# Kernel optimization log

Measured on AMD Instinct MI355X. Metric: run time of the kernel, lower is better.

## Reference

```python
import jax, jax.numpy as jnp
import numpy as np

B, NC, N, D_N, ALPHA = 8, 32, 128, 64, 4
HS, HM, HMOD = 128, 128, 64
MOD_IN = 2 * D_N + 5          # 133
MOD_OUT = N * N + N           # 16512


def setup_inputs() -> dict:
    key = jax.random.key(0)
    ks = jax.random.split(key, 16)
    f = jax.random.normal
    eye = jnp.eye(N, dtype=jnp.float32)
    return {
        "x": f(ks[0], (B, NC * D_N), jnp.float32),
        "h": f(ks[1], (B, NC, N, D_N), jnp.float32) * 0.01,
        "msg": f(ks[2], (B, NC, N, D_N), jnp.float32) * 0.1,
        "W": jnp.abs(f(ks[3], (B, NC, N, N), jnp.float32)) * 0.05 * (1.0 - eye),
        "decay_logit": f(ks[4], (B, NC, N), jnp.float32) * 0.1,
        "readout_drift": f(ks[5], (B, NC, 1), jnp.float32) * 0.1,
        "s_mem_live": f(ks[6], (B,), jnp.float32) * 0.1,
        "s_mem_ema_fast": f(ks[7], (B,), jnp.float32) * 0.1,
        "neuron_id": f(ks[8], (NC, N, D_N), jnp.float32) * 0.02,
        "state_w1": f(ks[9], (HS, 2 * D_N), jnp.float32) / np.sqrt(2 * D_N),
        "state_b1": jnp.zeros((HS,), jnp.float32),
        "state_w2": f(ks[10], (D_N, HS), jnp.float32) * 0.1 / np.sqrt(HS),
        "state_b2": jnp.zeros((D_N,), jnp.float32),
        "msg_w1": f(ks[11], (HM, D_N), jnp.float32) / np.sqrt(D_N),
        "msg_b1": jnp.zeros((HM,), jnp.float32),
        "msg_w2": f(ks[12], (D_N, HM), jnp.float32) * 0.1 / np.sqrt(HM),
        "msg_b2": jnp.zeros((D_N,), jnp.float32),
        "inject_w": f(ks[13], (NC, ALPHA * D_N, D_N), jnp.float32) / np.sqrt(D_N),
        "inject_b": jnp.zeros((NC, ALPHA * D_N), jnp.float32),
        "mod_w1": f(ks[14], (NC, MOD_IN, HMOD), jnp.float32) / np.sqrt(MOD_IN),
        "mod_b1": jnp.zeros((NC, HMOD), jnp.float32),
        "mod_w2": f(ks[15], (NC, HMOD, MOD_OUT), jnp.float32) * 0.01 / np.sqrt(HMOD),
        "mod_b2": jnp.zeros((NC, MOD_OUT), jnp.float32),
    }


def reference(x, h, msg, W, decay_logit, readout_drift, s_mem_live, s_mem_ema_fast,
              neuron_id, state_w1, state_b1, state_w2, state_b2,
              msg_w1, msg_b1, msg_w2, msg_b2, inject_w, inject_b,
              mod_w1, mod_b1, mod_w2, mod_b2):
    # --- message receive: dense per-cell adjacency matmul ---
    decay = jax.nn.sigmoid(decay_logit)[..., None]            # (B,NC,N,1)
    received = jnp.einsum('bcnm,bcmd->bcnd', W, msg)          # (B,NC,N,D_n)
    # --- inject external input into the alpha input-port neurons ---
    cell = x.reshape(B, NC, D_N)
    inj = jnp.einsum('bci,coi->bco', cell, inject_w) + inject_b   # (B,NC,alpha*D_n)
    received = received.at[:, :, :ALPHA].add(inj.reshape(B, NC, ALPHA, D_N))
    # --- state MLP with split first layer (avoids cat([received, h])) ---
    w1_recv, w1_h = state_w1[:, :D_N], state_w1[:, D_N:]
    hidden = jnp.tanh(jnp.einsum('bcnd,hd->bcnh', received, w1_recv)
                      + jnp.einsum('bcnd,hd->bcnh', h, w1_h) + state_b1)
    cand = jnp.tanh(jnp.einsum('bcnh,dh->bcnd', hidden, state_w2) + state_b2)
    h_new = decay * h + (1.0 - decay) * cand
    # --- emit message ---
    mh = jnp.tanh(jnp.einsum('bcnd,hd->bcnh', h_new, msg_w1) + msg_b1)
    msg_new = jnp.tanh(jnp.einsum('bcnh,dh->bcnd', mh, msg_w2) + msg_b2) + neuron_id[None]
    # --- readout from alpha output-port neurons ---
    readout = msg_new[:, :, ALPHA:2 * ALPHA].sum(axis=2) * (ALPHA ** -0.5)  # (B,NC,D_n)
    readout_flat = readout.reshape(B, NC * D_N)
    # --- per-cell modulator (stats -> tanh MLP -> delta_W, delta_decay) ---
    h_mean = h_new.mean(axis=2)                               # (B,NC,D_n)
    msg_mean = msg_new.mean(axis=2)
    W_stats = jnp.abs(W).mean(axis=-1).mean(axis=2, keepdims=True)  # (B,NC,1)
    decay_mean = decay_logit.mean(axis=2, keepdims=True)
    s1 = jnp.broadcast_to(s_mem_live[:, None, None], (B, NC, 1))
    s2 = jnp.broadcast_to(s_mem_ema_fast[:, None, None], (B, NC, 1))
    mod_input = jnp.concatenate([h_mean, msg_mean, W_stats, decay_mean,
                                 readout_drift, s1, s2], axis=-1)      # (B,NC,2*D_n+5)
    hid = jnp.tanh(jnp.einsum('bci,cih->bch', mod_input, mod_w1) + mod_b1)
    outm = jnp.einsum('bch,cho->bco', hid, mod_w2) + mod_b2            # (B,NC,N*N+N)
    delta_W = outm[..., :N * N].reshape(B, NC, N, N)
    delta_decay = outm[..., N * N:]
    eye = jnp.eye(N, dtype=W.dtype)
    W_new = (W + delta_W) * (1.0 - eye)   # additive modulation, no self-edges
    decay_new = decay_logit + delta_decay
    return readout_flat, h_new, msg_new, W_new, decay_new
```

## Files before the change

kernel.cpp:

```cpp
#include <hip/hip_runtime.h>
#include <math.h>


#define OUT_RO   0u
#define OUT_H    16384u
#define OUT_MSG  2113536u
#define OUT_W    4210688u
#define OUT_DEC  8404992u

#define TID ((int)threadIdx.x)

__device__ __forceinline__ float tanh_f(float v){ return tanhf(v); }

__global__ __launch_bounds__(256, 1)
void k1_cell(const float* __restrict__ x,
             const float* __restrict__ hg,
             const float* __restrict__ msgg,
             const float* __restrict__ Wg,
             const float* __restrict__ decay_logit,
             const float* __restrict__ readout_drift,
             const float* __restrict__ s_mem_live,
             const float* __restrict__ s_mem_ema_fast,
             const float* __restrict__ neuron_id,
             const float* __restrict__ state_w1,
             const float* __restrict__ state_b1,
             const float* __restrict__ state_w2,
             const float* __restrict__ state_b2,
             const float* __restrict__ msg_w1,
             const float* __restrict__ msg_b1,
             const float* __restrict__ msg_w2,
             const float* __restrict__ msg_b2,
             const float* __restrict__ inject_w,
             const float* __restrict__ inject_b,
             const float* __restrict__ mod_w1,
             const float* __restrict__ mod_b1,
             float* __restrict__ out,
             float* __restrict__ hid_ws)
{
    __shared__ __align__(16) float sD[128*132];
    __shared__ __align__(16) float sA[128*68];
    __shared__ __align__(16) float sB[128*68];
    __shared__ __align__(16) float s_b1[128];
    __shared__ __align__(16) float s_mb1[128];
    __shared__ __align__(16) float s_b2[64];
    __shared__ __align__(16) float s_mb2[64];
    __shared__ __align__(16) float s_cell[64];
    __shared__ __align__(16) float s_dlog[128];
    __shared__ __align__(16) float s_dec[128];
    __shared__ __align__(16) float s_modin[136];
    __shared__ __align__(16) float s_scr[16*68];
    __shared__ float s_wpart[4];

    const int bid = blockIdx.x;
    const int b   = bid >> 5;
    const int c   = bid & 31;
    const int ty  = TID >> 4;
    const int tx  = TID & 15;
    const int d4  = tx * 4;

    float wabs = 0.f;
    {
        const float4* src = (const float4*)(Wg + (size_t)bid * 16384);
        #pragma unroll
        for (int it = 0; it < 16; ++it) {
            int f4i = TID + it * 256;
            float4 v = src[f4i];
            int n = f4i >> 5, k = (f4i & 31) << 2;
            *(float4*)&sD[n*132 + k] = v;
            wabs += fabsf(v.x) + fabsf(v.y) + fabsf(v.z) + fabsf(v.w);
        }
    }
    {
        const float4* src = (const float4*)(msgg + (size_t)bid * 8192);
        #pragma unroll
        for (int it = 0; it < 8; ++it) {
            int f4i = TID + it * 256;
            float4 v = src[f4i];
            int n = f4i >> 4, d = (f4i & 15) << 2;
            *(float4*)&sA[n*68 + d] = v;
        }
    }
    {
        const float4* src = (const float4*)(hg + (size_t)bid * 8192);
        #pragma unroll
        for (int it = 0; it < 8; ++it) {
            int f4i = TID + it * 256;
            float4 v = src[f4i];
            int n = f4i >> 4, d = (f4i & 15) << 2;
            *(float4*)&sB[n*68 + d] = v;
        }
    }
    if (TID < 128) {
        s_b1[TID]  = state_b1[TID];
        s_mb1[TID] = msg_b1[TID];
        float dl = decay_logit[(size_t)bid*128 + TID];
        s_dlog[TID] = dl;
        s_dec[TID]  = 1.f / (1.f + expf(-dl));
    }
    if (TID < 64) {
        s_b2[TID]   = state_b2[TID];
        s_mb2[TID]  = msg_b2[TID];
        s_cell[TID] = x[(size_t)b*2048 + c*64 + TID];
    }
    #pragma unroll
    for (int off = 32; off > 0; off >>= 1) wabs += __shfl_down(wabs, off);
    if ((TID & 63) == 0) s_wpart[TID >> 6] = wabs;

    __syncthreads();

    float4 acc[8];
    #pragma unroll
    for (int i = 0; i < 8; ++i) acc[i] = make_float4(0.f,0.f,0.f,0.f);
    #pragma unroll 4
    for (int k = 0; k < 128; ++k) {
        float4 m4 = *(const float4*)&sA[k*68 + d4];
        #pragma unroll
        for (int i = 0; i < 8; ++i) {
            float w = sD[(ty + 16*i)*132 + k];
            acc[i].x += w * m4.x; acc[i].y += w * m4.y;
            acc[i].z += w * m4.z; acc[i].w += w * m4.w;
        }
    }
    __syncthreads();

    #pragma unroll
    for (int i = 0; i < 8; ++i)
        *(float4*)&sA[(ty + 16*i)*68 + d4] = acc[i];
    {
        const float4* src = (const float4*)state_w1;
        #pragma unroll
        for (int it = 0; it < 16; ++it) {
            int f4i = TID + it * 256;
            float4 v = src[f4i];
            int n = f4i >> 5, k = (f4i & 31) << 2;
            *(float4*)&sD[n*132 + k] = v;
        }
    }
    if (TID == 0) {
        float ws_ = (s_wpart[0] + s_wpart[1] + s_wpart[2] + s_wpart[3]) * (1.f/16384.f);
        float ds = 0.f;
        for (int n = 0; n < 128; ++n) ds += s_dlog[n];
        s_modin[128] = ws_;
        s_modin[129] = ds * (1.f/128.f);
        s_modin[130] = readout_drift[bid];
        s_modin[131] = s_mem_live[b];
        s_modin[132] = s_mem_ema_fast[b];
    }
    __syncthreads();

    {
        int o = TID;
        float s = inject_b[(size_t)c*256 + o];
        const float4* iw = (const float4*)(inject_w + (size_t)c*16384 + (size_t)o*64);
        #pragma unroll 4
        for (int q = 0; q < 16; ++q) {
            float4 w4 = iw[q];
            float4 cl = *(const float4*)&s_cell[q*4];
            s += w4.x*cl.x + w4.y*cl.y + w4.z*cl.z + w4.w*cl.w;
        }
        sA[(o >> 6)*68 + (o & 63)] += s;
    }
    __syncthreads();

    {
        float acc2[8][8];
        #pragma unroll
        for (int i = 0; i < 8; ++i)
            #pragma unroll
            for (int j = 0; j < 8; ++j) acc2[i][j] = 0.f;
        #pragma unroll 2
        for (int k = 0; k < 64; ++k) {
            float rv[8], hv[8], wr[8], wh[8];
            #pragma unroll
            for (int i = 0; i < 8; ++i) {
                int n = ty + 16*i;
                rv[i] = sA[n*68 + k];
                hv[i] = sB[n*68 + k];
            }
            #pragma unroll
            for (int j = 0; j < 8; ++j) {
                int hh = tx + 16*j;
                wr[j] = sD[hh*132 + k];
                wh[j] = sD[hh*132 + 64 + k];
            }
            #pragma unroll
            for (int i = 0; i < 8; ++i)
                #pragma unroll
                for (int j = 0; j < 8; ++j)
                    acc2[i][j] += rv[i]*wr[j] + hv[i]*wh[j];
        }
        __syncthreads();
        #pragma unroll
        for (int i = 0; i < 8; ++i)
            #pragma unroll
            for (int j = 0; j < 8; ++j)
                sD[(ty + 16*i)*132 + (tx + 16*j)] = tanh_f(acc2[i][j] + s_b1[tx + 16*j]);
    }
    {
        const float4* src = (const float4*)state_w2;
        #pragma unroll
        for (int it = 0; it < 8; ++it) {
            int f4i = TID + it * 256;
            float4 v = src[f4i];
            int d = f4i >> 5, hh = (f4i & 31) << 2;
            sA[(hh+0)*68 + d] = v.x;
            sA[(hh+1)*68 + d] = v.y;
            sA[(hh+2)*68 + d] = v.z;
            sA[(hh+3)*68 + d] = v.w;
        }
    }
    __syncthreads();

    {
        #pragma unroll
        for (int i = 0; i < 8; ++i) acc[i] = make_float4(0.f,0.f,0.f,0.f);
        #pragma unroll 4
        for (int k = 0; k < 128; ++k) {
            float4 w4 = *(const float4*)&sA[k*68 + d4];
            #pragma unroll
            for (int i = 0; i < 8; ++i) {
                float hv = sD[(ty + 16*i)*132 + k];
                acc[i].x += hv * w4.x; acc[i].y += hv * w4.y;
                acc[i].z += hv * w4.z; acc[i].w += hv * w4.w;
            }
        }
        float4 b2v = *(const float4*)&s_b2[d4];
        float4 hpart = make_float4(0.f,0.f,0.f,0.f);
        #pragma unroll
        for (int i = 0; i < 8; ++i) {
            int n = ty + 16*i;
            float dec = s_dec[n];
            float4 hold = *(const float4*)&sB[n*68 + d4];
            float4 hn;
            hn.x = dec*hold.x + (1.f-dec)*tanh_f(acc[i].x + b2v.x);
            hn.y = dec*hold.y + (1.f-dec)*tanh_f(acc[i].y + b2v.y);
            hn.z = dec*hold.z + (1.f-dec)*tanh_f(acc[i].z + b2v.z);
            hn.w = dec*hold.w + (1.f-dec)*tanh_f(acc[i].w + b2v.w);
            *(float4*)&sB[n*68 + d4] = hn;
            *(float4*)(out + OUT_H + (size_t)bid*8192 + n*64 + d4) = hn;
            hpart.x += hn.x; hpart.y += hn.y; hpart.z += hn.z; hpart.w += hn.w;
        }
        *(float4*)&s_scr[ty*68 + d4] = hpart;
    }
    __syncthreads();
    if (TID < 64) {
        float s = 0.f;
        #pragma unroll
        for (int t = 0; t < 16; ++t) s += s_scr[t*68 + TID];
        s_modin[TID] = s * (1.f/128.f);
    }
    {
        const float4* src = (const float4*)msg_w1;
        #pragma unroll
        for (int it = 0; it < 8; ++it) {
            int f4i = TID + it * 256;
            float4 v = src[f4i];
            int hh = f4i >> 4, d = (f4i & 15) << 2;
            *(float4*)&sA[hh*68 + d] = v;
        }
    }
    __syncthreads();

    {
        float acc2[8][8];
        #pragma unroll
        for (int i = 0; i < 8; ++i)
            #pragma unroll
            for (int j = 0; j < 8; ++j) acc2[i][j] = 0.f;
        #pragma unroll 2
        for (int k = 0; k < 64; ++k) {
            float hv[8], wv[8];
            #pragma unroll
            for (int i = 0; i < 8; ++i) hv[i] = sB[(ty + 16*i)*68 + k];
            #pragma unroll
            for (int j = 0; j < 8; ++j) wv[j] = sA[(tx + 16*j)*68 + k];
            #pragma unroll
            for (int i = 0; i < 8; ++i)
                #pragma unroll
                for (int j = 0; j < 8; ++j)
                    acc2[i][j] += hv[i]*wv[j];
        }
        __syncthreads();
        #pragma unroll
        for (int i = 0; i < 8; ++i)
            #pragma unroll
            for (int j = 0; j < 8; ++j)
                sD[(ty + 16*i)*132 + (tx + 16*j)] = tanh_f(acc2[i][j] + s_mb1[tx + 16*j]);
    }
    {
        const float4* src = (const float4*)msg_w2;
        #pragma unroll
        for (int it = 0; it < 8; ++it) {
            int f4i = TID + it * 256;
            float4 v = src[f4i];
            int d = f4i >> 5, hh = (f4i & 31) << 2;
            sA[(hh+0)*68 + d] = v.x;
            sA[(hh+1)*68 + d] = v.y;
            sA[(hh+2)*68 + d] = v.z;
            sA[(hh+3)*68 + d] = v.w;
        }
    }
    __syncthreads();

    {
        #pragma unroll
        for (int i = 0; i < 8; ++i) acc[i] = make_float4(0.f,0.f,0.f,0.f);
        #pragma unroll 4
        for (int k = 0; k < 128; ++k) {
            float4 w4 = *(const float4*)&sA[k*68 + d4];
            #pragma unroll
            for (int i = 0; i < 8; ++i) {
                float mv = sD[(ty + 16*i)*132 + k];
                acc[i].x += mv * w4.x; acc[i].y += mv * w4.y;
                acc[i].z += mv * w4.z; acc[i].w += mv * w4.w;
            }
        }
        float4 mb2 = *(const float4*)&s_mb2[d4];
        float4 mpart = make_float4(0.f,0.f,0.f,0.f);
        #pragma unroll
        for (int i = 0; i < 8; ++i) {
            int n = ty + 16*i;
            float4 nid = *(const float4*)(neuron_id + (size_t)c*8192 + n*64 + d4);
            float4 mn;
            mn.x = tanh_f(acc[i].x + mb2.x) + nid.x;
            mn.y = tanh_f(acc[i].y + mb2.y) + nid.y;
            mn.z = tanh_f(acc[i].z + mb2.z) + nid.z;
            mn.w = tanh_f(acc[i].w + mb2.w) + nid.w;
            *(float4*)&sB[n*68 + d4] = mn;
            *(float4*)(out + OUT_MSG + (size_t)bid*8192 + n*64 + d4) = mn;
            mpart.x += mn.x; mpart.y += mn.y; mpart.z += mn.z; mpart.w += mn.w;
        }
        *(float4*)&s_scr[ty*68 + d4] = mpart;
    }
    __syncthreads();
    if (TID < 64) {
        float s = 0.f;
        #pragma unroll
        for (int t = 0; t < 16; ++t) s += s_scr[t*68 + TID];
        s_modin[64 + TID] = s * (1.f/128.f);
        float r = (sB[4*68 + TID] + sB[5*68 + TID] + sB[6*68 + TID] + sB[7*68 + TID]) * 0.5f;
        out[OUT_RO + (size_t)b*2048 + c*64 + TID] = r;
    }
    __syncthreads();

    if (TID < 64) {
        int hh = TID;
        float a = mod_b1[(size_t)c*64 + hh];
        const float* w1p = mod_w1 + (size_t)c*8512 + hh;
        #pragma unroll 7
        for (int i = 0; i < 133; ++i)
            a += s_modin[i] * w1p[(size_t)i*64];
        hid_ws[(size_t)bid*64 + hh] = tanh_f(a);
    }
}

__global__ __launch_bounds__(512, 1)
void k2_wnew(const float* __restrict__ hid_ws,
             const float* __restrict__ mod_w2,
             const float* __restrict__ mod_b2,
             const float* __restrict__ Wg,
             const float* __restrict__ decay_logit,
             float* __restrict__ out)
{
    __shared__ float shid[512];
    const int c    = blockIdx.x >> 3;
    const int part = blockIdx.x & 7;

    shid[TID] = hid_ws[((size_t)((TID >> 6) * 32 + c))*64 + (TID & 63)];
    __syncthreads();

    for (int idx = TID; idx < 516; idx += 512) {
        int o = part * 2064 + idx * 4;
        float4 acc0[8];
        {
            float4 bv = *(const float4*)(mod_b2 + (size_t)c*16512 + o);
            #pragma unroll
            for (int bb = 0; bb < 8; ++bb) acc0[bb] = bv;
        }
        const float* w2p = mod_w2 + (size_t)c*1056768 + o;
        #pragma unroll 8
        for (int hh = 0; hh < 64; ++hh) {
            float4 w4 = *(const float4*)(w2p + (size_t)hh*16512);
            #pragma unroll
            for (int bb = 0; bb < 8; ++bb) {
                float hv = shid[bb*64 + hh];
                acc0[bb].x += hv * w4.x; acc0[bb].y += hv * w4.y;
                acc0[bb].z += hv * w4.z; acc0[bb].w += hv * w4.w;
            }
        }
        if (o < 16384) {
            int n = o >> 7, m = o & 127;
            #pragma unroll
            for (int bb = 0; bb < 8; ++bb) {
                size_t wof = ((size_t)(bb*32 + c) << 14) + o;
                float4 Wv = *(const float4*)(Wg + wof);
                float4 r;
                r.x = Wv.x + acc0[bb].x;
                r.y = Wv.y + acc0[bb].y;
                r.z = Wv.z + acc0[bb].z;
                r.w = Wv.w + acc0[bb].w;
                if (n == m)     r.x = 0.f;
                else if (n == m+1) r.y = 0.f;
                else if (n == m+2) r.z = 0.f;
                else if (n == m+3) r.w = 0.f;
                *(float4*)(out + OUT_W + wof) = r;
            }
        } else {
            int m = o - 16384;
            #pragma unroll
            for (int bb = 0; bb < 8; ++bb) {
                size_t dof = (size_t)(bb*32 + c)*128 + m;
                float4 dl = *(const float4*)(decay_logit + dof);
                float4 r;
                r.x = dl.x + acc0[bb].x;
                r.y = dl.y + acc0[bb].y;
                r.z = dl.z + acc0[bb].z;
                r.w = dl.w + acc0[bb].w;
                *(float4*)(out + OUT_DEC + dof) = r;
            }
        }
    }
}

extern "C" void kernel_launch(void* const* d_in, const int* in_sizes, int n_in,
                              void* d_out, int out_size, void* d_ws, size_t ws_size,
                              hipStream_t stream)
{
    (void)in_sizes; (void)n_in; (void)out_size; (void)ws_size;
    const float* x              = (const float*)d_in[0];
    const float* h              = (const float*)d_in[1];
    const float* msg            = (const float*)d_in[2];
    const float* W              = (const float*)d_in[3];
    const float* decay_logit    = (const float*)d_in[4];
    const float* readout_drift  = (const float*)d_in[5];
    const float* s_mem_live     = (const float*)d_in[6];
    const float* s_mem_ema_fast = (const float*)d_in[7];
    const float* neuron_id      = (const float*)d_in[8];
    const float* state_w1       = (const float*)d_in[9];
    const float* state_b1       = (const float*)d_in[10];
    const float* state_w2       = (const float*)d_in[11];
    const float* state_b2       = (const float*)d_in[12];
    const float* msg_w1         = (const float*)d_in[13];
    const float* msg_b1         = (const float*)d_in[14];
    const float* msg_w2         = (const float*)d_in[15];
    const float* msg_b2         = (const float*)d_in[16];
    const float* inject_w       = (const float*)d_in[17];
    const float* inject_b       = (const float*)d_in[18];
    const float* mod_w1         = (const float*)d_in[19];
    const float* mod_b1         = (const float*)d_in[20];
    const float* mod_w2         = (const float*)d_in[21];
    const float* mod_b2         = (const float*)d_in[22];

    float* out = (float*)d_out;
    float* ws  = (float*)d_ws;

    hipLaunchKernelGGL(k1_cell, dim3(256), dim3(256), 0, stream,
                       x, h, msg, W, decay_logit, readout_drift,
                       s_mem_live, s_mem_ema_fast, neuron_id,
                       state_w1, state_b1, state_w2, state_b2,
                       msg_w1, msg_b1, msg_w2, msg_b2,
                       inject_w, inject_b, mod_w1, mod_b1,
                       out, ws);

    hipLaunchKernelGGL(k2_wnew, dim3(256), dim3(512), 0, stream,
                       ws, mod_w2, mod_b2, W, decay_logit, out);
}
```

Before: 371.3 us.

## Rewrite cell kernel with bf16 MFMA matmuls and rebalance modulator grid

New measurement: 312.4 us. 15.9% less time.

```diff
diff --git a/kernel.cpp b/kernel.cpp
--- a/kernel.cpp
+++ b/kernel.cpp
@@ -8,11 +8,27 @@
 #define OUT_W    4210688u
 #define OUT_DEC  8404992u
 
-#define TID ((int)threadIdx.x)
-
-__device__ __forceinline__ float tanh_f(float v){ return tanhf(v); }
-
-__global__ __launch_bounds__(256, 1)
+typedef __bf16 bf16x8 __attribute__((ext_vector_type(8)));
+typedef float  f32x4  __attribute__((ext_vector_type(4)));
+
+__device__ __forceinline__ unsigned short bf16_rne(float f){
+    unsigned int u = __float_as_uint(f);
+    u += 0x7fffu + ((u >> 16) & 1u);
+    return (unsigned short)(u >> 16);
+}
+__device__ __forceinline__ float bf16_f(unsigned short s){
+    return __uint_as_float(((unsigned int)s) << 16);
+}
+__device__ __forceinline__ float tanh_fast(float x){
+    float e = __expf(2.f * x);
+    return 1.f - 2.f / (e + 1.f);
+}
+__device__ __forceinline__ bf16x8 frag(const unsigned short* p, int row, int stride, int kbyte){
+    return *(const bf16x8*)((const char*)(p + row * stride) + kbyte);
+}
+#define MFMA16(a, b, c) __builtin_amdgcn_mfma_f32_16x16x32_bf16(a, b, c, 0, 0, 0)
+
+__global__ __launch_bounds__(512)
 void k1_cell(const float* __restrict__ x,
              const float* __restrict__ hg,
              const float* __restrict__ msgg,
@@ -37,324 +53,374 @@
              float* __restrict__ out,
              float* __restrict__ hid_ws)
 {
-    __shared__ __align__(16) float sD[128*132];
-    __shared__ __align__(16) float sA[128*68];
-    __shared__ __align__(16) float sB[128*68];
-    __shared__ __align__(16) float s_b1[128];
-    __shared__ __align__(16) float s_mb1[128];
-    __shared__ __align__(16) float s_b2[64];
-    __shared__ __align__(16) float s_mb2[64];
-    __shared__ __align__(16) float s_cell[64];
-    __shared__ __align__(16) float s_dlog[128];
-    __shared__ __align__(16) float s_dec[128];
-    __shared__ __align__(16) float s_modin[136];
-    __shared__ __align__(16) float s_scr[16*68];
-    __shared__ float s_wpart[4];
-
-    const int bid = blockIdx.x;
-    const int b   = bid >> 5;
-    const int c   = bid & 31;
-    const int ty  = TID >> 4;
-    const int tx  = TID & 15;
-    const int d4  = tx * 4;
+    __shared__ __align__(16) unsigned short sW[128*136];
+    __shared__ __align__(16) unsigned short sM[64*136];
+    __shared__ __align__(16) unsigned short sR[128*72];
+    __shared__ __align__(16) unsigned short sH[128*72];
+    __shared__ __align__(16) float scrH[32*64];
+    __shared__ __align__(16) float scrM[32*64];
+    __shared__ __align__(16) float s_inj[256];
+    __shared__ float s_b1[128], s_mb1[128], s_b2[64], s_mb2[64];
+    __shared__ float s_cell[64], s_dlog[128], s_dec[128];
+    __shared__ float s_modin[136];
+    __shared__ float s_wpart[8];
+
+    const int tid  = (int)threadIdx.x;
+    const int bid  = (int)blockIdx.x;
+    const int b    = bid >> 5, c = bid & 31;
+    const int wid  = tid >> 6, lane = tid & 63;
+    const int q    = lane >> 4, r16 = lane & 15;
+    const int wm   = wid >> 1, wn = wid & 1;
+    const int ar   = wm*32 + r16;
 
     float wabs = 0.f;
     {
         const float4* src = (const float4*)(Wg + (size_t)bid * 16384);
         #pragma unroll
-        for (int it = 0; it < 16; ++it) {
-            int f4i = TID + it * 256;
-            float4 v = src[f4i];
-            int n = f4i >> 5, k = (f4i & 31) << 2;
-            *(float4*)&sD[n*132 + k] = v;
-            wabs += fabsf(v.x) + fabsf(v.y) + fabsf(v.z) + fabsf(v.w);
+        for (int it = 0; it < 8; ++it) {
+            int f4i = tid + it*512;
+            float4 v = src[f4i];
+            int n = f4i >> 5, k4 = (f4i & 31) << 2;
+            ushort4 u;
+            u.x = bf16_rne(v.x); u.y = bf16_rne(v.y);
+            u.z = bf16_rne(v.z); u.w = bf16_rne(v.w);
+            *(ushort4*)&sW[n*136 + k4] = u;
+            wabs += fabsf(v.x)+fabsf(v.y)+fabsf(v.z)+fabsf(v.w);
         }
     }
     {
         const float4* src = (const float4*)(msgg + (size_t)bid * 8192);
         #pragma unroll
-        for (int it = 0; it < 8; ++it) {
-            int f4i = TID + it * 256;
-            float4 v = src[f4i];
-            int n = f4i >> 4, d = (f4i & 15) << 2;
-            *(float4*)&sA[n*68 + d] = v;
+        for (int it = 0; it < 4; ++it) {
+            int f4i = tid + it*512;
+            float4 v = src[f4i];
+            int m = f4i >> 4, d4 = (f4i & 15) << 2;
+            sM[(d4+0)*136 + m] = bf16_rne(v.x);
+            sM[(d4+1)*136 + m] = bf16_rne(v.y);
+            sM[(d4+2)*136 + m] = bf16_rne(v.z);
+            sM[(d4+3)*136 + m] = bf16_rne(v.w);
         }
     }
     {
         const float4* src = (const float4*)(hg + (size_t)bid * 8192);
         #pragma unroll
-        for (int it = 0; it < 8; ++it) {
-            int f4i = TID + it * 256;
-            float4 v = src[f4i];
-            int n = f4i >> 4, d = (f4i & 15) << 2;
-            *(float4*)&sB[n*68 + d] = v;
-        }
-    }
-    if (TID < 128) {
-        s_b1[TID]  = state_b1[TID];
-        s_mb1[TID] = msg_b1[TID];
-        float dl = decay_logit[(size_t)bid*128 + TID];
-        s_dlog[TID] = dl;
-        s_dec[TID]  = 1.f / (1.f + expf(-dl));
-    }
-    if (TID < 64) {
-        s_b2[TID]   = state_b2[TID];
-        s_mb2[TID]  = msg_b2[TID];
-        s_cell[TID] = x[(size_t)b*2048 + c*64 + TID];
-    }
-    #pragma unroll
-    for (int off = 32; off > 0; off >>= 1) wabs += __shfl_down(wabs, off);
-    if ((TID & 63) == 0) s_wpart[TID >> 6] = wabs;
-
-    __syncthreads();
-
-    float4 acc[8];
-    #pragma unroll
-    for (int i = 0; i < 8; ++i) acc[i] = make_float4(0.f,0.f,0.f,0.f);
-    #pragma unroll 4
-    for (int k = 0; k < 128; ++k) {
-        float4 m4 = *(const float4*)&sA[k*68 + d4];
-        #pragma unroll
-        for (int i = 0; i < 8; ++i) {
-            float w = sD[(ty + 16*i)*132 + k];
-            acc[i].x += w * m4.x; acc[i].y += w * m4.y;
-            acc[i].z += w * m4.z; acc[i].w += w * m4.w;
-        }
-    }
-    __syncthreads();
-
-    #pragma unroll
-    for (int i = 0; i < 8; ++i)
-        *(float4*)&sA[(ty + 16*i)*68 + d4] = acc[i];
-    {
-        const float4* src = (const float4*)state_w1;
-        #pragma unroll
-        for (int it = 0; it < 16; ++it) {
-            int f4i = TID + it * 256;
-            float4 v = src[f4i];
-            int n = f4i >> 5, k = (f4i & 31) << 2;
-            *(float4*)&sD[n*132 + k] = v;
-        }
-    }
-    if (TID == 0) {
-        float ws_ = (s_wpart[0] + s_wpart[1] + s_wpart[2] + s_wpart[3]) * (1.f/16384.f);
+        for (int it = 0; it < 4; ++it) {
+            int f4i = tid + it*512;
+            float4 v = src[f4i];
+            int n = f4i >> 4, d4 = (f4i & 15) << 2;
+            ushort4 u;
+            u.x = bf16_rne(v.x); u.y = bf16_rne(v.y);
+            u.z = bf16_rne(v.z); u.w = bf16_rne(v.w);
+            *(ushort4*)&sH[n*72 + d4] = u;
+        }
+    }
+    if (tid < 128) {
+        s_b1[tid]  = state_b1[tid];
+        s_mb1[tid] = msg_b1[tid];
+        float dl = decay_logit[(size_t)bid*128 + tid];
+        s_dlog[tid] = dl;
+        s_dec[tid]  = 1.f / (1.f + __expf(-dl));
+    }
+    if (tid < 64) {
+        s_b2[tid]  = state_b2[tid];
+        s_mb2[tid] = msg_b2[tid];
+        s_cell[tid] = x[(size_t)b*2048 + c*64 + tid];
+    }
+    #pragma unroll
+    for (int off = 32; off; off >>= 1) wabs += __shfl_down(wabs, off);
+    if (lane == 0) s_wpart[wid] = wabs;
+
+    __syncthreads();
+
+    if (tid < 256) {
+        int o = tid;
+        float s = inject_b[(size_t)c*256 + o];
+        const float4* iw = (const float4*)(inject_w + (size_t)c*16384 + (size_t)o*64);
+        #pragma unroll
+        for (int qq = 0; qq < 16; ++qq) {
+            float4 w4 = iw[qq];
+            float4 cl = *(const float4*)&s_cell[qq*4];
+            s += w4.x*cl.x + w4.y*cl.y + w4.z*cl.z + w4.w*cl.w;
+        }
+        s_inj[o] = s;
+    }
+    if (tid == 0) {
+        float ws_ = 0.f;
+        #pragma unroll
+        for (int i = 0; i < 8; ++i) ws_ += s_wpart[i];
         float ds = 0.f;
         for (int n = 0; n < 128; ++n) ds += s_dlog[n];
-        s_modin[128] = ws_;
+        s_modin[128] = ws_ * (1.f/16384.f);
         s_modin[129] = ds * (1.f/128.f);
         s_modin[130] = readout_drift[bid];
         s_modin[131] = s_mem_live[b];
         s_modin[132] = s_mem_ema_fast[b];
     }
-    __syncthreads();
-
-    {
-        int o = TID;
-        float s = inject_b[(size_t)c*256 + o];
-        const float4* iw = (const float4*)(inject_w + (size_t)c*16384 + (size_t)o*64);
-        #pragma unroll 4
-        for (int q = 0; q < 16; ++q) {
-            float4 w4 = iw[q];
-            float4 cl = *(const float4*)&s_cell[q*4];
-            s += w4.x*cl.x + w4.y*cl.y + w4.z*cl.z + w4.w*cl.w;
-        }
-        sA[(o >> 6)*68 + (o & 63)] += s;
-    }
-    __syncthreads();
-
-    {
-        float acc2[8][8];
-        #pragma unroll
-        for (int i = 0; i < 8; ++i)
-            #pragma unroll
-            for (int j = 0; j < 8; ++j) acc2[i][j] = 0.f;
-        #pragma unroll 2
-        for (int k = 0; k < 64; ++k) {
-            float rv[8], hv[8], wr[8], wh[8];
-            #pragma unroll
-            for (int i = 0; i < 8; ++i) {
-                int n = ty + 16*i;
-                rv[i] = sA[n*68 + k];
-                hv[i] = sB[n*68 + k];
-            }
-            #pragma unroll
-            for (int j = 0; j < 8; ++j) {
-                int hh = tx + 16*j;
-                wr[j] = sD[hh*132 + k];
-                wh[j] = sD[hh*132 + 64 + k];
-            }
-            #pragma unroll
-            for (int i = 0; i < 8; ++i)
-                #pragma unroll
-                for (int j = 0; j < 8; ++j)
-                    acc2[i][j] += rv[i]*wr[j] + hv[i]*wh[j];
-        }
-        __syncthreads();
-        #pragma unroll
-        for (int i = 0; i < 8; ++i)
-            #pragma unroll
-            for (int j = 0; j < 8; ++j)
-                sD[(ty + 16*i)*132 + (tx + 16*j)] = tanh_f(acc2[i][j] + s_b1[tx + 16*j]);
+
+    f32x4 a1[2][2];
+    #pragma unroll
+    for (int i = 0; i < 2; ++i)
+        #pragma unroll
+        for (int j = 0; j < 2; ++j) a1[i][j] = (f32x4){0.f,0.f,0.f,0.f};
+    #pragma unroll
+    for (int ks = 0; ks < 4; ++ks) {
+        int kb = ks*64 + q*16;
+        bf16x8 A0 = frag(sW, ar,      136, kb);
+        bf16x8 A1 = frag(sW, ar+16,   136, kb);
+        bf16x8 B0 = frag(sM, wn*32 + r16,      136, kb);
+        bf16x8 B1 = frag(sM, wn*32 + 16 + r16, 136, kb);
+        a1[0][0] = MFMA16(A0, B0, a1[0][0]);
+        a1[0][1] = MFMA16(A0, B1, a1[0][1]);
+        a1[1][0] = MFMA16(A1, B0, a1[1][0]);
+        a1[1][1] = MFMA16(A1, B1, a1[1][1]);
+    }
+    __syncthreads();
+
+    #pragma unroll
+    for (int i = 0; i < 2; ++i)
+        #pragma unroll
+        for (int j = 0; j < 2; ++j) {
+            int colb = wn*32 + j*16 + r16;
+            #pragma unroll
+            for (int r = 0; r < 4; ++r) {
+                int row = wm*32 + i*16 + q*4 + r;
+                float v = a1[i][j][r];
+                if (row < 4) { v += s_inj[row*64 + colb]; }
+                sR[row*72 + colb] = bf16_rne(v);
+            }
+        }
+    {
+        const float4* src = (const float4*)state_w1;
+        #pragma unroll
+        for (int it = 0; it < 8; ++it) {
+            int f4i = tid + it*512;
+            float4 v = src[f4i];
+            int n = f4i >> 5, k4 = (f4i & 31) << 2;
+            ushort4 u;
+            u.x = bf16_rne(v.x); u.y = bf16_rne(v.y);
+            u.z = bf16_rne(v.z); u.w = bf16_rne(v.w);
+            *(ushort4*)&sW[n*136 + k4] = u;
+        }
     }
     {
         const float4* src = (const float4*)state_w2;
         #pragma unroll
-        for (int it = 0; it < 8; ++it) {
-            int f4i = TID + it * 256;
-            float4 v = src[f4i];
-            int d = f4i >> 5, hh = (f4i & 31) << 2;
-            sA[(hh+0)*68 + d] = v.x;
-            sA[(hh+1)*68 + d] = v.y;
-            sA[(hh+2)*68 + d] = v.z;
-            sA[(hh+3)*68 + d] = v.w;
-        }
-    }
-    __syncthreads();
-
-    {
-        #pragma unroll
-        for (int i = 0; i < 8; ++i) acc[i] = make_float4(0.f,0.f,0.f,0.f);
-        #pragma unroll 4
-        for (int k = 0; k < 128; ++k) {
-            float4 w4 = *(const float4*)&sA[k*68 + d4];
-            #pragma unroll
-            for (int i = 0; i < 8; ++i) {
-                float hv = sD[(ty + 16*i)*132 + k];
-                acc[i].x += hv * w4.x; acc[i].y += hv * w4.y;
-                acc[i].z += hv * w4.z; acc[i].w += hv * w4.w;
-            }
-        }
-        float4 b2v = *(const float4*)&s_b2[d4];
-        float4 hpart = make_float4(0.f,0.f,0.f,0.f);
-        #pragma unroll
-        for (int i = 0; i < 8; ++i) {
-            int n = ty + 16*i;
-            float dec = s_dec[n];
-            float4 hold = *(const float4*)&sB[n*68 + d4];
-            float4 hn;
-            hn.x = dec*hold.x + (1.f-dec)*tanh_f(acc[i].x + b2v.x);
-            hn.y = dec*hold.y + (1.f-dec)*tanh_f(acc[i].y + b2v.y);
-            hn.z = dec*hold.z + (1.f-dec)*tanh_f(acc[i].z + b2v.z);
-            hn.w = dec*hold.w + (1.f-dec)*tanh_f(acc[i].w + b2v.w);
-            *(float4*)&sB[n*68 + d4] = hn;
-            *(float4*)(out + OUT_H + (size_t)bid*8192 + n*64 + d4) = hn;
-            hpart.x += hn.x; hpart.y += hn.y; hpart.z += hn.z; hpart.w += hn.w;
-        }
-        *(float4*)&s_scr[ty*68 + d4] = hpart;
-    }
-    __syncthreads();
-    if (TID < 64) {
-        float s = 0.f;
-        #pragma unroll
-        for (int t = 0; t < 16; ++t) s += s_scr[t*68 + TID];
-        s_modin[TID] = s * (1.f/128.f);
-    }
+        for (int it = 0; it < 4; ++it) {
+            int f4i = tid + it*512;
+            float4 v = src[f4i];
+            int n = f4i >> 5, k4 = (f4i & 31) << 2;
+            ushort4 u;
+            u.x = bf16_rne(v.x); u.y = bf16_rne(v.y);
+            u.z = bf16_rne(v.z); u.w = bf16_rne(v.w);
+            *(ushort4*)&sM[n*136 + k4] = u;
+        }
+    }
+    __syncthreads();
+
+    f32x4 a2[2][4];
+    #pragma unroll
+    for (int i = 0; i < 2; ++i)
+        #pragma unroll
+        for (int j = 0; j < 4; ++j) a2[i][j] = (f32x4){0.f,0.f,0.f,0.f};
+    #pragma unroll
+    for (int ks = 0; ks < 2; ++ks) {
+        int kb = ks*64 + q*16;
+        bf16x8 A0 = frag(sR, ar,    72, kb);
+        bf16x8 A1 = frag(sR, ar+16, 72, kb);
+        #pragma unroll
+        for (int j = 0; j < 4; ++j) {
+            bf16x8 Bj = frag(sW, wn*64 + j*16 + r16, 136, kb);
+            a2[0][j] = MFMA16(A0, Bj, a2[0][j]);
+            a2[1][j] = MFMA16(A1, Bj, a2[1][j]);
+        }
+    }
+    #pragma unroll
+    for (int ks = 0; ks < 2; ++ks) {
+        int kb = ks*64 + q*16;
+        bf16x8 A0 = frag(sH, ar,    72, kb);
+        bf16x8 A1 = frag(sH, ar+16, 72, kb);
+        #pragma unroll
+        for (int j = 0; j < 4; ++j) {
+            bf16x8 Bj = frag(sW, wn*64 + j*16 + r16, 136, 128 + kb);
+            a2[0][j] = MFMA16(A0, Bj, a2[0][j]);
+            a2[1][j] = MFMA16(A1, Bj, a2[1][j]);
+        }
+    }
+    __syncthreads();
+
+    #pragma unroll
+    for (int i = 0; i < 2; ++i)
+        #pragma unroll
+        for (int j = 0; j < 4; ++j) {
+            int colb = wn*64 + j*16 + r16;
+            float bb = s_b1[colb];
+            #pragma unroll
+            for (int r = 0; r < 4; ++r) {
+                int row = wm*32 + i*16 + q*4 + r;
+                sW[row*136 + colb] = bf16_rne(tanh_fast(a2[i][j][r] + bb));
+            }
+        }
     {
         const float4* src = (const float4*)msg_w1;
         #pragma unroll
-        for (int it = 0; it < 8; ++it) {
-            int f4i = TID + it * 256;
-            float4 v = src[f4i];
-            int hh = f4i >> 4, d = (f4i & 15) << 2;
-            *(float4*)&sA[hh*68 + d] = v;
-        }
-    }
-    __syncthreads();
-
-    {
-        float acc2[8][8];
-        #pragma unroll
-        for (int i = 0; i < 8; ++i)
-            #pragma unroll
-            for (int j = 0; j < 8; ++j) acc2[i][j] = 0.f;
-        #pragma unroll 2
-        for (int k = 0; k < 64; ++k) {
-            float hv[8], wv[8];
-            #pragma unroll
-            for (int i = 0; i < 8; ++i) hv[i] = sB[(ty + 16*i)*68 + k];
-            #pragma unroll
-            for (int j = 0; j < 8; ++j) wv[j] = sA[(tx + 16*j)*68 + k];
-            #pragma unroll
-            for (int i = 0; i < 8; ++i)
-                #pragma unroll
-                for (int j = 0; j < 8; ++j)
-                    acc2[i][j] += hv[i]*wv[j];
-        }
-        __syncthreads();
-        #pragma unroll
-        for (int i = 0; i < 8; ++i)
-            #pragma unroll
-            for (int j = 0; j < 8; ++j)
-                sD[(ty + 16*i)*132 + (tx + 16*j)] = tanh_f(acc2[i][j] + s_mb1[tx + 16*j]);
-    }
+        for (int it = 0; it < 4; ++it) {
+            int f4i = tid + it*512;
+            float4 v = src[f4i];
+            int n = f4i >> 4, d4 = (f4i & 15) << 2;
+            ushort4 u;
+            u.x = bf16_rne(v.x); u.y = bf16_rne(v.y);
+            u.z = bf16_rne(v.z); u.w = bf16_rne(v.w);
+            *(ushort4*)&sR[n*72 + d4] = u;
+        }
+    }
+    __syncthreads();
+
+    f32x4 a3[2][2];
+    #pragma unroll
+    for (int i = 0; i < 2; ++i)
+        #pragma unroll
+        for (int j = 0; j < 2; ++j) a3[i][j] = (f32x4){0.f,0.f,0.f,0.f};
+    #pragma unroll
+    for (int ks = 0; ks < 4; ++ks) {
+        int kb = ks*64 + q*16;
+        bf16x8 A0 = frag(sW, ar,    136, kb);
+        bf16x8 A1 = frag(sW, ar+16, 136, kb);
+        bf16x8 B0 = frag(sM, wn*32 + r16,      136, kb);
+        bf16x8 B1 = frag(sM, wn*32 + 16 + r16, 136, kb);
+        a3[0][0] = MFMA16(A0, B0, a3[0][0]);
+        a3[0][1] = MFMA16(A0, B1, a3[0][1]);
+        a3[1][0] = MFMA16(A1, B0, a3[1][0]);
+        a3[1][1] = MFMA16(A1, B1, a3[1][1]);
+    }
+    #pragma unroll
+    for (int i = 0; i < 2; ++i)
+        #pragma unroll
+        for (int j = 0; j < 2; ++j) {
+            int colb = wn*32 + j*16 + r16;
+            float b2v = s_b2[colb];
+            float psum = 0.f;
+            #pragma unroll
+            for (int r = 0; r < 4; ++r) {
+                int row = wm*32 + i*16 + q*4 + r;
+                float cand = tanh_fast(a3[i][j][r] + b2v);
+                float hold = bf16_f(sH[row*72 + colb]);
+                float dec  = s_dec[row];
+                float hn   = dec*hold + (1.f - dec)*cand;
+                out[OUT_H + (size_t)bid*8192 + row*64 + colb] = hn;
+                sH[row*72 + colb] = bf16_rne(hn);
+                psum += hn;
+            }
+            scrH[((wm*2 + i)*4 + q)*64 + colb] = psum;
+        }
+    __syncthreads();
+
     {
         const float4* src = (const float4*)msg_w2;
         #pragma unroll
-        for (int it = 0; it < 8; ++it) {
-            int f4i = TID + it * 256;
-            float4 v = src[f4i];
-            int d = f4i >> 5, hh = (f4i & 31) << 2;
-            sA[(hh+0)*68 + d] = v.x;
-            sA[(hh+1)*68 + d] = v.y;
-            sA[(hh+2)*68 + d] = v.z;
-            sA[(hh+3)*68 + d] = v.w;
-        }
-    }
-    __syncthreads();
-
-    {
-        #pragma unroll
-        for (int i = 0; i < 8; ++i) acc[i] = make_float4(0.f,0.f,0.f,0.f);
-        #pragma unroll 4
-        for (int k = 0; k < 128; ++k) {
-            float4 w4 = *(const float4*)&sA[k*68 + d4];
-            #pragma unroll
-            for (int i = 0; i < 8; ++i) {
-                float mv = sD[(ty + 16*i)*132 + k];
-                acc[i].x += mv * w4.x; acc[i].y += mv * w4.y;
-                acc[i].z += mv * w4.z; acc[i].w += mv * w4.w;
-            }
-        }
-        float4 mb2 = *(const float4*)&s_mb2[d4];
-        float4 mpart = make_float4(0.f,0.f,0.f,0.f);
-        #pragma unroll
-        for (int i = 0; i < 8; ++i) {
-            int n = ty + 16*i;
-            float4 nid = *(const float4*)(neuron_id + (size_t)c*8192 + n*64 + d4);
-            float4 mn;
-            mn.x = tanh_f(acc[i].x + mb2.x) + nid.x;
-            mn.y = tanh_f(acc[i].y + mb2.y) + nid.y;
-            mn.z = tanh_f(acc[i].z + mb2.z) + nid.z;
-            mn.w = tanh_f(acc[i].w + mb2.w) + nid.w;
-            *(float4*)&sB[n*68 + d4] = mn;
-            *(float4*)(out + OUT_MSG + (size_t)bid*8192 + n*64 + d4) = mn;
-            mpart.x += mn.x; mpart.y += mn.y; mpart.z += mn.z; mpart.w += mn.w;
-        }
-        *(float4*)&s_scr[ty*68 + d4] = mpart;
-    }
-    __syncthreads();
-    if (TID < 64) {
-        float s = 0.f;
-        #pragma unroll
-        for (int t = 0; t < 16; ++t) s += s_scr[t*68 + TID];
-        s_modin[64 + TID] = s * (1.f/128.f);
-        float r = (sB[4*68 + TID] + sB[5*68 + TID] + sB[6*68 + TID] + sB[7*68 + TID]) * 0.5f;
-        out[OUT_RO + (size_t)b*2048 + c*64 + TID] = r;
-    }
-    __syncthreads();
-
-    if (TID < 64) {
-        int hh = TID;
+        for (int it = 0; it < 4; ++it) {
+            int f4i = tid + it*512;
+            float4 v = src[f4i];
+            int n = f4i >> 5, k4 = (f4i & 31) << 2;
+            ushort4 u;
+            u.x = bf16_rne(v.x); u.y = bf16_rne(v.y);
+            u.z = bf16_rne(v.z); u.w = bf16_rne(v.w);
+            *(ushort4*)&sM[n*136 + k4] = u;
+        }
+    }
+
+    f32x4 a4[2][4];
+    #pragma unroll
+    for (int i = 0; i < 2; ++i)
+        #pragma unroll
+        for (int j = 0; j < 4; ++j) a4[i][j] = (f32x4){0.f,0.f,0.f,0.f};
+    #pragma unroll
+    for (int ks = 0; ks < 2; ++ks) {
+        int kb = ks*64 + q*16;
+        bf16x8 A0 = frag(sH, ar,    72, kb);
+        bf16x8 A1 = frag(sH, ar+16, 72, kb);
+        #pragma unroll
+        for (int j = 0; j < 4; ++j) {
+            bf16x8 Bj = frag(sR, wn*64 + j*16 + r16, 72, kb);
+            a4[0][j] = MFMA16(A0, Bj, a4[0][j]);
+            a4[1][j] = MFMA16(A1, Bj, a4[1][j]);
+        }
+    }
+    #pragma unroll
+    for (int i = 0; i < 2; ++i)
+        #pragma unroll
+        for (int j = 0; j < 4; ++j) {
+            int colb = wn*64 + j*16 + r16;
+            float bb = s_mb1[colb];
+            #pragma unroll
+            for (int r = 0; r < 4; ++r) {
+                int row = wm*32 + i*16 + q*4 + r;
+                sW[row*136 + colb] = bf16_rne(tanh_fast(a4[i][j][r] + bb));
+            }
+        }
+    __syncthreads();
+
+    f32x4 a5[2][2];
+    #pragma unroll
+    for (int i = 0; i < 2; ++i)
+        #pragma unroll
+        for (int j = 0; j < 2; ++j) a5[i][j] = (f32x4){0.f,0.f,0.f,0.f};
+    #pragma unroll
+    for (int ks = 0; ks < 4; ++ks) {
+        int kb = ks*64 + q*16;
+        bf16x8 A0 = frag(sW, ar,    136, kb);
+        bf16x8 A1 = frag(sW, ar+16, 136, kb);
+        bf16x8 B0 = frag(sM, wn*32 + r16,      136, kb);
+        bf16x8 B1 = frag(sM, wn*32 + 16 + r16, 136, kb);
+        a5[0][0] = MFMA16(A0, B0, a5[0][0]);
+        a5[0][1] = MFMA16(A0, B1, a5[0][1]);
+        a5[1][0] = MFMA16(A1, B0, a5[1][0]);
+        a5[1][1] = MFMA16(A1, B1, a5[1][1]);
+    }
+    #pragma unroll
+    for (int i = 0; i < 2; ++i)
+        #pragma unroll
+        for (int j = 0; j < 2; ++j) {
+            int colb = wn*32 + j*16 + r16;
+            float mb = s_mb2[colb];
+            float psum = 0.f;
+            float rosum = 0.f;
+            #pragma unroll
+            for (int r = 0; r < 4; ++r) {
+                int row = wm*32 + i*16 + q*4 + r;
+                float nid = neuron_id[(size_t)c*8192 + row*64 + colb];
+                float mn = tanh_fast(a5[i][j][r] + mb) + nid;
+                out[OUT_MSG + (size_t)bid*8192 + row*64 + colb] = mn;
+                psum += mn;
+                rosum += mn;
+            }
+            scrM[((wm*2 + i)*4 + q)*64 + colb] = psum;
+            if (wm == 0 && i == 0 && q == 1) {
+                out[OUT_RO + (size_t)b*2048 + c*64 + colb] = 0.5f * rosum;
+            }
+        }
+    __syncthreads();
+
+    if (tid < 64) {
+        float hm = 0.f, mm = 0.f;
+        #pragma unroll
+        for (int g = 0; g < 32; ++g) { hm += scrH[g*64 + tid]; mm += scrM[g*64 + tid]; }
+        s_modin[tid]      = hm * (1.f/128.f);
+        s_modin[64 + tid] = mm * (1.f/128.f);
+    }
+    __syncthreads();
+
+    if (tid < 64) {
+        int hh = tid;
         float a = mod_b1[(size_t)c*64 + hh];
         const float* w1p = mod_w1 + (size_t)c*8512 + hh;
         #pragma unroll 7
         for (int i = 0; i < 133; ++i)
             a += s_modin[i] * w1p[(size_t)i*64];
-        hid_ws[(size_t)bid*64 + hh] = tanh_f(a);
-    }
-}
-
-__global__ __launch_bounds__(512, 1)
+        hid_ws[(size_t)bid*64 + hh] = tanh_fast(a);
+    }
+}
+
+__global__ __launch_bounds__(256)
 void k2_wnew(const float* __restrict__ hid_ws,
              const float* __restrict__ mod_w2,
              const float* __restrict__ mod_b2,
@@ -362,62 +428,91 @@
              const float* __restrict__ decay_logit,
              float* __restrict__ out)
 {
-    __shared__ float shid[512];
-    const int c    = blockIdx.x >> 3;
-    const int part = blockIdx.x & 7;
-
-    shid[TID] = hid_ws[((size_t)((TID >> 6) * 32 + c))*64 + (TID & 63)];
-    __syncthreads();
-
-    for (int idx = TID; idx < 516; idx += 512) {
-        int o = part * 2064 + idx * 4;
-        float4 acc0[8];
+    __shared__ float shid[4096];
+    const int tid = (int)threadIdx.x;
+
+    if ((int)blockIdx.x < 512) {
+        const int c = (int)blockIdx.x >> 4, part = (int)blockIdx.x & 15;
+        shid[tid]       = hid_ws[(size_t)((tid>>6)*32 + c)*64 + (tid&63)];
+        shid[tid + 256] = hid_ws[(size_t)(((tid>>6)+4)*32 + c)*64 + (tid&63)];
+        __syncthreads();
+
+        const int o = (part*256 + tid) * 4;
+        float4 acc[8];
         {
             float4 bv = *(const float4*)(mod_b2 + (size_t)c*16512 + o);
             #pragma unroll
-            for (int bb = 0; bb < 8; ++bb) acc0[bb] = bv;
+            for (int bb = 0; bb < 8; ++bb) acc[bb] = bv;
         }
         const float* w2p = mod_w2 + (size_t)c*1056768 + o;
-        #pragma unroll 8
+        #pragma unroll 16
         for (int hh = 0; hh < 64; ++hh) {
             float4 w4 = *(const float4*)(w2p + (size_t)hh*16512);
             #pragma unroll
             for (int bb = 0; bb < 8; ++bb) {
                 float hv = shid[bb*64 + hh];
-                acc0[bb].x += hv * w4.x; acc0[bb].y += hv * w4.y;
-                acc0[bb].z += hv * w4.z; acc0[bb].w += hv * w4.w;
-            }
-        }
-        if (o < 16384) {
-            int n = o >> 7, m = o & 127;
+                acc[bb].x += hv * w4.x; acc[bb].y += hv * w4.y;
+                acc[bb].z += hv * w4.z; acc[bb].w += hv * w4.w;
+            }
+        }
+        const int n = o >> 7, m = o & 127;
+        #pragma unroll
+        for (int bb = 0; bb < 8; ++bb) {
+            size_t wof = ((size_t)(bb*32 + c) << 14) + o;
+            float4 Wv = *(const float4*)(Wg + wof);
+            float4 r;
+            r.x = Wv.x + acc[bb].x;
+            r.y = Wv.y + acc[bb].y;
+            r.z = Wv.z + acc[bb].z;
+            r.w = Wv.w + acc[bb].w;
+            if (n == m)        r.x = 0.f;
+            else if (n == m+1) r.y = 0.f;
+            else if (n == m+2) r.z = 0.f;
+            else if (n == m+3) r.w = 0.f;
+            *(float4*)(out + OUT_W + wof) = r;
+        }
+    } else {
+        const int base_c = ((int)blockIdx.x - 512) * 8;
+        #pragma unroll
+        for (int it = 0; it < 16; ++it) {
+            int idx = tid + it*256;
+            int c_l = idx >> 9, rem = idx & 511;
+            int bb = rem >> 6, h = rem & 63;
+            shid[idx] = hid_ws[(size_t)(bb*32 + base_c + c_l)*64 + h];
+        }
+        __syncthreads();
+
+        const int c_l = tid >> 5;
+        const int c   = base_c + c_l;
+        const int m4  = (tid & 31) * 4;
+        const int o   = 16384 + m4;
+        float4 acc[8];
+        {
+            float4 bv = *(const float4*)(mod_b2 + (size_t)c*16512 + o);
+            #pragma unroll
+            for (int bb = 0; bb < 8; ++bb) acc[bb] = bv;
+        }
+        const float* w2p = mod_w2 + (size_t)c*1056768 + o;
+        #pragma unroll 16
+        for (int hh = 0; hh < 64; ++hh) {
+            float4 w4 = *(const float4*)(w2p + (size_t)hh*16512);
             #pragma unroll
             for (int bb = 0; bb < 8; ++bb) {
-                size_t wof = ((size_t)(bb*32 + c) << 14) + o;
-                float4 Wv = *(const float4*)(Wg + wof);
-                float4 r;
-                r.x = Wv.x + acc0[bb].x;
-                r.y = Wv.y + acc0[bb].y;
-                r.z = Wv.z + acc0[bb].z;
-                r.w = Wv.w + acc0[bb].w;
-                if (n == m)     r.x = 0.f;
-                else if (n == m+1) r.y = 0.f;
-                else if (n == m+2) r.z = 0.f;
-                else if (n == m+3) r.w = 0.f;
-                *(float4*)(out + OUT_W + wof) = r;
-            }
-        } else {
-            int m = o - 16384;
-            #pragma unroll
-            for (int bb = 0; bb < 8; ++bb) {
-                size_t dof = (size_t)(bb*32 + c)*128 + m;
-                float4 dl = *(const float4*)(decay_logit + dof);
-                float4 r;
-                r.x = dl.x + acc0[bb].x;
-                r.y = dl.y + acc0[bb].y;
-                r.z = dl.z + acc0[bb].z;
-                r.w = dl.w + acc0[bb].w;
-                *(float4*)(out + OUT_DEC + dof) = r;
-            }
+                float hv = shid[c_l*512 + bb*64 + hh];
+                acc[bb].x += hv * w4.x; acc[bb].y += hv * w4.y;
+                acc[bb].z += hv * w4.z; acc[bb].w += hv * w4.w;
+            }
+        }
+        #pragma unroll
+        for (int bb = 0; bb < 8; ++bb) {
+            size_t dof = (size_t)(bb*32 + c)*128 + m4;
+            float4 dl = *(const float4*)(decay_logit + dof);
+            float4 r;
+            r.x = dl.x + acc[bb].x;
+            r.y = dl.y + acc[bb].y;
+            r.z = dl.z + acc[bb].z;
+            r.w = dl.w + acc[bb].w;
+            *(float4*)(out + OUT_DEC + dof) = r;
         }
     }
 }
@@ -454,7 +549,7 @@
     float* out = (float*)d_out;
     float* ws  = (float*)d_ws;
 
-    hipLaunchKernelGGL(k1_cell, dim3(256), dim3(256), 0, stream,
+    hipLaunchKernelGGL(k1_cell, dim3(256), dim3(512), 0, stream,
                        x, h, msg, W, decay_logit, readout_drift,
                        s_mem_live, s_mem_ema_fast, neuron_id,
                        state_w1, state_b1, state_w2, state_b2,
@@ -462,6 +557,6 @@
                        inject_w, inject_b, mod_w1, mod_b1,
                        out, ws);
 
-    hipLaunchKernelGGL(k2_wnew, dim3(256), dim3(512), 0, stream,
+    hipLaunchKernelGGL(k2_wnew, dim3(516), dim3(256), 0, stream,
                        ws, mod_w2, mod_b2, W, decay_logit, out);
 }
```
